# Optimization experiments

Measured on AMD Instinct MI355X. Metric: run time of the kernel, lower is better.

## Reference

```python
import jax, jax.numpy as jnp
import numpy as np
from jax import lax

PRE_NMS_TOPN = 6000
POST_NMS_TOPN = 300
NMS_IOU = 0.7
VARIANCES = np.array([0.1, 0.1, 0.2, 0.2], dtype=np.float32)


def setup_inputs() -> dict:
    key = jax.random.key(0)
    k1, k2, k3, k4 = jax.random.split(key, 4)
    B, FH, FW, K = 32, 128, 128, 9
    A = FH * FW * K  # 147456 total anchors
    rpn_bbox_deltas = jax.random.normal(k1, (B, A, 4), dtype=jnp.float32) * 0.1
    rpn_labels = jax.random.normal(k2, (B, FH, FW, K), dtype=jnp.float32)
    # Anchors in [y1, x1, y2, x2] with y1<y2, x1<x2 on a ~1024px image.
    ctr = jax.random.uniform(k3, (A, 2), dtype=jnp.float32) * 1024.0
    wh = jax.random.uniform(k4, (A, 2), dtype=jnp.float32) * 224.0 + 32.0
    anchors = jnp.concatenate([ctr - 0.5 * wh, ctr + 0.5 * wh], axis=-1)
    return {"rpn_bbox_deltas": rpn_bbox_deltas, "rpn_labels": rpn_labels, "anchors": anchors}


def get_bboxes_from_deltas(anchors, deltas):
    # anchors: [A, 4] (y1,x1,y2,x2); deltas: [B, A, 4] (dy,dx,dh,dw)
    anc_w = anchors[..., 3] - anchors[..., 1]
    anc_h = anchors[..., 2] - anchors[..., 0]
    anc_cx = anchors[..., 1] + 0.5 * anc_w
    anc_cy = anchors[..., 0] + 0.5 * anc_h
    bb_w = jnp.exp(deltas[..., 3]) * anc_w
    bb_h = jnp.exp(deltas[..., 2]) * anc_h
    bb_cx = deltas[..., 1] * anc_w + anc_cx
    bb_cy = deltas[..., 0] * anc_h + anc_cy
    y1 = bb_cy - 0.5 * bb_h
    x1 = bb_cx - 0.5 * bb_w
    y2 = bb_h + y1
    x2 = bb_w + x1
    return jnp.stack([y1, x1, y2, x2], axis=-1)


def nms_per_image(boxes, scores, iou_threshold, num_keep):
    # boxes: [N, 4] sorted by descending score; scores: [N]
    y1, x1, y2, x2 = boxes[:, 0], boxes[:, 1], boxes[:, 2], boxes[:, 3]
    areas = (y2 - y1) * (x2 - x1)

    def step(scores_rem, _):
        idx = jnp.argmax(scores_rem)
        valid = jnp.isfinite(scores_rem[idx])
        b = boxes[idx]
        iy1 = jnp.maximum(b[0], y1)
        ix1 = jnp.maximum(b[1], x1)
        iy2 = jnp.minimum(b[2], y2)
        ix2 = jnp.minimum(b[3], x2)
        inter = jnp.clip(iy2 - iy1, 0.0) * jnp.clip(ix2 - ix1, 0.0)
        b_area = (b[2] - b[0]) * (b[3] - b[1])
        iou = inter / (areas + b_area - inter + 1e-9)
        # IoU(box, itself) == 1 > threshold, so the picked box is also suppressed.
        new_scores = jnp.where(iou > iou_threshold, -jnp.inf, scores_rem)
        return new_scores, (idx, valid)

    _, (keep_idx, valid) = lax.scan(step, scores, None, length=num_keep)
    vf = valid.astype(boxes.dtype)
    keep_boxes = boxes[keep_idx] * vf[:, None]  # zero-pad invalid slots
    keep_scores = scores[keep_idx] * vf
    return keep_boxes, keep_scores


def reference(rpn_bbox_deltas, rpn_labels, anchors):
    A = anchors.shape[0]
    B = rpn_bbox_deltas.shape[0]
    deltas = rpn_bbox_deltas.reshape(B, A, 4) * jnp.asarray(VARIANCES)
    labels = jax.nn.softmax(rpn_labels, axis=-1).reshape(B, A)
    rpn_bboxes = get_bboxes_from_deltas(anchors, deltas)  # [B, A, 4]
    # top-k pre-NMS filter (lax.top_k output is already sorted descending)
    pre_scores, pre_idx = lax.top_k(labels, PRE_NMS_TOPN)  # [B, P]
    pre_boxes = jnp.take_along_axis(rpn_bboxes, pre_idx[..., None], axis=1)  # [B, P, 4]
    nms_fn = lambda b, s: nms_per_image(b, s, NMS_IOU, POST_NMS_TOPN)
    roi_bboxes, roi_scores = jax.vmap(nms_fn)(pre_boxes, pre_scores)
    return roi_bboxes, roi_scores
```

## Files before the change

kernel.cpp:

```cpp
#include <hip/hip_runtime.h>
#include <cstdint>
#include <cstddef>

#pragma clang fp contract(off)

#define KCLS 9
#define PRE_N 6000
#define POST_N 300
#define NMS_IOU_T 0.7f
#define HIST_BLOCK 256
#define CHUNKS_PER_IMG 32
#define NMS_BLOCK 512
#define NSEG 8
#define SEG_CAP 2048
#define RANK_LDS 8192

#define SUPP(pb, pa, mbx, mar, out) \
    bool out; { \
        float iy1_ = fmaxf((pb).x, (mbx).x); \
        float ix1_ = fmaxf((pb).y, (mbx).y); \
        float iy2_ = fminf((pb).z, (mbx).z); \
        float ix2_ = fminf((pb).w, (mbx).w); \
        float ih_ = iy2_ - iy1_; ih_ = ih_ > 0.f ? ih_ : 0.f; \
        float iw_ = ix2_ - ix1_; iw_ = iw_ > 0.f ? iw_ : 0.f; \
        float inter_ = ih_ * iw_; \
        float den_ = (mar) + (pa) - inter_ + 1e-9f; \
        float hi_ = 0.7000007f * den_; \
        float lo_ = 0.6999993f * den_; \
        out = inter_ > hi_; \
        if (inter_ >= lo_ && inter_ <= hi_) out = (inter_ / den_) > NMS_IOU_T; \
    }

__device__ __forceinline__ void pick_dev(
        const unsigned int* __restrict__ gh,
        int shift, int bins,
        unsigned int prefix_in, unsigned int krem_in,
        unsigned int* cnt,
        unsigned int* ssum,
        unsigned int* out) {
    const int t = threadIdx.x;
    const int per = bins >> 8;
    unsigned int my = 0;
    if (t < 256) {
        for (int i = 0; i < per; ++i) {
            unsigned int c = gh[t * per + i];
            cnt[t * per + i] = c;
            my += c;
        }
        ssum[t] = my;
    }
    __syncthreads();
    for (int d = 1; d < 256; d <<= 1) {
        unsigned int v = 0u;
        if (t < 256 && t + d < 256) v = ssum[t + d];
        __syncthreads();
        if (t < 256) ssum[t] += v;
        __syncthreads();
    }
    if (t < 256) {
        unsigned int above = ssum[t] - my;
        if (above < krem_in && ssum[t] >= krem_in) {
            unsigned int cum = above;
            for (int b = per - 1; b >= 0; --b) {
                unsigned int c = cnt[t * per + b];
                if (cum + c >= krem_in) {
                    out[0] = prefix_in | ((unsigned int)(t * per + b) << shift);
                    out[1] = krem_in - cum;
                    break;
                }
                cum += c;
            }
        }
    }
    __syncthreads();
}

__global__ void __launch_bounds__(256)
softmax_hist_kernel(const float* __restrict__ labels,
                    float* __restrict__ scores,
                    unsigned int* __restrict__ ghist,
                    int gpi) {
    __shared__ float buf[256 * KCLS];
    __shared__ unsigned int h[2048 * 4];
    const int tid = threadIdx.x;
    for (int i = tid; i < 2048 * 4; i += 256) h[i] = 0u;

    const size_t gbase = (size_t)blockIdx.x * (256 * KCLS);
    const float4* lin4 = (const float4*)(labels + gbase);
    float4* b4 = (float4*)buf;
    for (int i = tid; i < 576; i += 256) b4[i] = lin4[i];
    __syncthreads();

    const int sub = tid & 3;
    float v[KCLS];
    float m = -1e30f;
    #pragma unroll
    for (int k = 0; k < KCLS; ++k) { v[k] = buf[tid * KCLS + k]; m = fmaxf(m, v[k]); }
    float e[KCLS];
    float s = 0.f;
    #pragma unroll
    for (int k = 0; k < KCLS; ++k) { e[k] = expf(v[k] - m); s += e[k]; }
    #pragma unroll
    for (int k = 0; k < KCLS; ++k) {
        float r = e[k] / s;
        buf[tid * KCLS + k] = r;
        atomicAdd(&h[(((__float_as_uint(r) >> 21) & 2047u) << 2) | sub], 1u);
    }
    __syncthreads();

    float4* o4 = (float4*)(scores + gbase);
    for (int i = tid; i < 576; i += 256) o4[i] = b4[i];

    const int img0 = (blockIdx.x * 256) / gpi;
    unsigned int* gh = ghist + (size_t)img0 * 2048;
    for (int i = tid; i < 2048; i += 256) {
        unsigned int c = h[4 * i] + h[4 * i + 1] + h[4 * i + 2] + h[4 * i + 3];
        if (c) atomicAdd(&gh[i], c);
    }
}

__global__ void __launch_bounds__(HIST_BLOCK)
hist2_kernel(const float* __restrict__ scores,
             const unsigned int* __restrict__ ghist1,
             unsigned int* __restrict__ ghist2,
             int A) {
    __shared__ unsigned int h[2048];
    __shared__ unsigned int ssum[256];
    __shared__ unsigned int pk[2];
    const int img = blockIdx.y;
    const int chunk = blockIdx.x;
    const int tid = threadIdx.x;

    pick_dev(ghist1 + (size_t)img * 2048, 21, 2048, 0u, (unsigned)PRE_N, h, ssum, pk);
    const unsigned int prefix = pk[0];

    for (int i = tid; i < 2048; i += HIST_BLOCK) h[i] = 0u;
    __syncthreads();
    const int per = A / CHUNKS_PER_IMG;
    const float* sc = scores + (size_t)img * A + (size_t)chunk * per;
    for (int i = tid; i < per; i += HIST_BLOCK) {
        unsigned int v = __float_as_uint(sc[i]);
        if ((v & 0xFFE00000u) == prefix)
            atomicAdd(&h[(v >> 10) & 2047u], 1u);
    }
    __syncthreads();
    unsigned int* gh = ghist2 + (size_t)img * 2048;
    for (int i = tid; i < 2048; i += HIST_BLOCK) {
        unsigned int c = h[i];
        if (c) atomicAdd(&gh[i], c);
    }
}

#define CE(a, b, u) { if ((v[a] > v[b]) == (u)) { unsigned long long t_ = v[a]; v[a] = v[b]; v[b] = t_; } }
#define REG3(u) { CE(0,4,u) CE(1,5,u) CE(2,6,u) CE(3,7,u) \
                  CE(0,2,u) CE(1,3,u) CE(4,6,u) CE(5,7,u) \
                  CE(0,1,u) CE(2,3,u) CE(4,5,u) CE(6,7,u) }

__global__ void __launch_bounds__(512)
compact_sort_kernel(const float* __restrict__ scores,
                    const unsigned int* __restrict__ ghist1,
                    const unsigned int* __restrict__ ghist2,
                    unsigned long long* __restrict__ pool,
                    unsigned int* __restrict__ counts,
                    int A) {
    __shared__ unsigned long long lin[SEG_CAP];
    __shared__ unsigned int plo[2][SEG_CAP];
    __shared__ unsigned int phi[2][SEG_CAP];
    __shared__ unsigned int ssum[256];
    __shared__ unsigned int pk[2];
    __shared__ unsigned int cnt;
    const int img = blockIdx.y;
    const int seg = blockIdx.x;
    const int tid = threadIdx.x;
    const int lane = tid & 63;
    const int w = tid >> 6;
    const float* sc = scores + (size_t)img * A;

    unsigned int* cnt32 = (unsigned int*)lin;
    pick_dev(ghist1 + (size_t)img * 2048, 21, 2048, 0u, (unsigned)PRE_N, cnt32, ssum, pk);
    const unsigned int p1 = pk[0];
    const unsigned int k1 = pk[1];
    pick_dev(ghist2 + (size_t)img * 2048, 10, 2048, p1, k1, cnt32, ssum, pk);
    const unsigned int T = pk[0];

    if (tid == 0) cnt = 0u;
    for (int i = tid; i < SEG_CAP; i += 512) lin[i] = ~0ull;
    __syncthreads();

    const int ngr = A >> 6;
    const int nj = ngr / NSEG;
    for (int j = w; j < nj; j += 8) {
        int g = seg + j * NSEG;
        int i = (g << 6) + lane;
        unsigned int sv = __float_as_uint(sc[i]);
        bool push = (sv >= T);
        unsigned long long bal = __ballot(push ? 1 : 0);
        if (push) {
            int leader = __ffsll(bal) - 1;
            int rank = __popcll(bal & ((1ull << lane) - 1ull));
            unsigned int base = 0;
            if (lane == leader) base = atomicAdd(&cnt, (unsigned int)__popcll(bal));
            base = (unsigned int)__shfl((int)base, leader);
            unsigned int pos = base + (unsigned int)rank;
            if (pos < SEG_CAP)
                lin[pos] = (((unsigned long long)(~sv)) << 32) | (unsigned long long)(unsigned int)i;
        }
    }
    __syncthreads();

    int n = (int)cnt; if (n > SEG_CAP) n = SEG_CAP;
    int P2 = 512; while (P2 < n) P2 <<= 1;
    const int NT = P2 >> 3;
    const int t = tid;
    const bool act = (t < NT);

    unsigned long long v[8];
    if (act) {
        #pragma unroll
        for (int e = 0; e < 8; ++e) v[e] = lin[(t << 3) + e];
        CE(0,1,true) CE(2,3,false) CE(4,5,true) CE(6,7,false)
        CE(0,2,true) CE(1,3,true) CE(4,6,false) CE(5,7,false)
        CE(0,1,true) CE(2,3,true) CE(4,5,false) CE(6,7,false)
        bool u8 = ((t & 1) == 0);
        REG3(u8)
    }
    int b = 0;
    for (int k = 16; k <= P2; k <<= 1) {
        const bool up = (((t << 3) & k) == 0);
        for (int j = k >> 1; j >= 8; j >>= 1) {
            const int c = j >> 3;
            if (act) {
                #pragma unroll
                for (int e = 0; e < 8; ++e) {
                    int idx = e * NT + t;
                    plo[b][idx] = (unsigned int)v[e];
                    phi[b][idx] = (unsigned int)(v[e] >> 32);
                }
            }
            __syncthreads();
            if (act) {
                const int q = t ^ c;
                const bool keep_min = (up == ((t & c) == 0));
                #pragma unroll
                for (int e = 0; e < 8; ++e) {
                    int idx = e * NT + q;
                    unsigned long long wv = ((unsigned long long)phi[b][idx] << 32)
                                          | (unsigned long long)plo[b][idx];
                    bool less = v[e] < wv;
                    v[e] = (less == keep_min) ? v[e] : wv;
                }
            }
            b ^= 1;
        }
        if (act) { REG3(up) }
    }

    unsigned long long* gp = pool + ((size_t)img * NSEG + seg) * SEG_CAP;
    if (act) {
        #pragma unroll
        for (int e = 0; e < 8; ++e) {
            int r = (t << 3) + e;
            if (r < n) gp[r] = v[e];
        }
    }
    if (tid == 0) counts[img * NSEG + seg] = (unsigned int)n;
}

__global__ void __launch_bounds__(256)
rank_decode_kernel(const unsigned long long* __restrict__ pool,
                   const unsigned int* __restrict__ counts,
                   const float* __restrict__ deltas,
                   const float* __restrict__ anchors,
                   float* __restrict__ pre_boxes,
                   float* __restrict__ pre_scores,
                   int A) {
    __shared__ unsigned long long arr[RANK_LDS];
    const int img = blockIdx.y;
    const int seg = blockIdx.x;
    const int tid = threadIdx.x;

    int c[NSEG], off[NSEG + 1];
    const unsigned long long* gp[NSEG];
    off[0] = 0;
    #pragma unroll
    for (int s = 0; s < NSEG; ++s) {
        int cs = (int)counts[img * NSEG + s];
        if (cs > SEG_CAP) cs = SEG_CAP;
        c[s] = cs;
        off[s + 1] = off[s] + cs;
        gp[s] = pool + ((size_t)img * NSEG + s) * SEG_CAP;
    }
    const int total = off[NSEG];
    const bool inlds = (total <= RANK_LDS);
    if (inlds) {
        #pragma unroll
        for (int s = 0; s < NSEG; ++s)
            for (int i = tid; i < c[s]; i += 256) arr[off[s] + i] = gp[s][i];
    }
    __syncthreads();

    const int m = c[seg];
    for (int i = tid; i < m; i += 256) {
        unsigned long long key = inlds ? arr[off[seg] + i] : gp[seg][i];
        int pos = i;
        #pragma unroll
        for (int s = 0; s < NSEG; ++s) {
            if (s == seg) continue;
            const unsigned long long* base = inlds ? (arr + off[s]) : gp[s];
            int lo = 0, hi = c[s];
            while (lo < hi) {
                int mid = (lo + hi) >> 1;
                if (base[mid] < key) lo = mid + 1; else hi = mid;
            }
            pos += lo;
        }
        if (pos < PRE_N) {
            unsigned int bidx = (unsigned int)(key & 0xFFFFFFFFull);
            unsigned int sbits = ~((unsigned int)(key >> 32));
            float score = __uint_as_float(sbits);
            float a0 = anchors[(size_t)bidx * 4 + 0];
            float a1 = anchors[(size_t)bidx * 4 + 1];
            float a2 = anchors[(size_t)bidx * 4 + 2];
            float a3 = anchors[(size_t)bidx * 4 + 3];
            const float* dd = deltas + ((size_t)img * A + bidx) * 4;
            float d0 = dd[0] * 0.1f;
            float d1 = dd[1] * 0.1f;
            float d2 = dd[2] * 0.2f;
            float d3 = dd[3] * 0.2f;
            float anc_w = a3 - a1;
            float anc_h = a2 - a0;
            float anc_cx = a1 + 0.5f * anc_w;
            float anc_cy = a0 + 0.5f * anc_h;
            float bb_w = expf(d3) * anc_w;
            float bb_h = expf(d2) * anc_h;
            float bb_cx = d1 * anc_w + anc_cx;
            float bb_cy = d0 * anc_h + anc_cy;
            float y1 = bb_cy - 0.5f * bb_h;
            float x1 = bb_cx - 0.5f * bb_w;
            float y2 = bb_h + y1;
            float x2 = bb_w + x1;
            float* ob = pre_boxes + ((size_t)img * PRE_N + pos) * 4;
            ob[0] = y1; ob[1] = x1; ob[2] = y2; ob[3] = x2;
            pre_scores[(size_t)img * PRE_N + pos] = score;
        }
    }
}

__global__ void __launch_bounds__(NMS_BLOCK)
nms_kernel(const float* __restrict__ pre_boxes,
           const float* __restrict__ pre_scores,
           float* __restrict__ out_boxes,
           float* __restrict__ out_scores) {
    const int img = blockIdx.x;
    const int tid = threadIdx.x;
    const int lane = tid & 63;
    const int grp = tid >> 6;
    const float4* bb4 = (const float4*)(pre_boxes + (size_t)img * PRE_N * 4);

    __shared__ float4 kept[POST_N];
    __shared__ float  kept_area[POST_N];
    __shared__ int    kept_idx[POST_N];
    __shared__ float4 chunkbox[2][64];
    __shared__ unsigned long long rows[64];
    __shared__ unsigned long long supball[8];
    __shared__ int kept_cnt;

    const int NCH = (PRE_N + 63) >> 6;

    float4 nb = make_float4(0.f, 0.f, 0.f, 0.f);
    if (tid < 64) {
        chunkbox[0][tid] = bb4[tid];
        nb = bb4[64 + tid];
    }
    if (tid == 0) kept_cnt = 0;
    __syncthreads();

    for (int c = 0; c < NCH; ++c) {
        const int base = c << 6;
        const int cur = c & 1;
        const int K = kept_cnt;
        float4 mb = chunkbox[cur][lane];
        float marea = (mb.z - mb.x) * (mb.w - mb.y);

        bool sup = false;
        for (int k = grp; k < K; k += 8) {
            float4 pb = kept[k];
            float pa = kept_area[k];
            SUPP(pb, pa, mb, marea, s)
            if (s) { sup = true; break; }
        }
        unsigned long long bal = __ballot(sup ? 1 : 0);
        if (lane == 0) supball[grp] = bal;

        #pragma unroll
        for (int u = 0; u < 8; ++u) {
            const int i = (grp << 3) + u;
            float4 pb = chunkbox[cur][i];
            float pa = (pb.z - pb.x) * (pb.w - pb.y);
            SUPP(pb, pa, mb, marea, s)
            unsigned long long rb = __ballot(s ? 1 : 0);
            if (lane == 0) rows[i] = rb;
        }

        if (tid < 64) {
            chunkbox[cur ^ 1][tid] = nb;
            int j = base + 128 + tid;
            nb = (j < PRE_N) ? bb4[j] : make_float4(0.f, 0.f, 0.f, 0.f);
        }
        __syncthreads();

        if (grp == 0) {
            const int remn = PRE_N - base;
            unsigned long long ext = (remn >= 64) ? ~0ull : ((1ull << remn) - 1ull);
            unsigned long long sb = supball[0] | supball[1] | supball[2] | supball[3]
                                  | supball[4] | supball[5] | supball[6] | supball[7];
            unsigned long long rem = ext & ~sb;
            unsigned long long myrow = rows[lane];
            int kc = K;
            while (rem && kc < POST_N) {
                const int i = __ffsll(rem) - 1;
                if (lane == i) {
                    kept[kc] = mb;
                    kept_area[kc] = marea;
                    kept_idx[kc] = base + i;
                }
                unsigned long long ri = __shfl(myrow, i);
                rem &= ~(1ull << i);
                rem &= ~ri;
                ++kc;
            }
            if (lane == 0) kept_cnt = kc;
        }
        __syncthreads();
        if (kept_cnt >= POST_N) break;
    }

    const int kc = kept_cnt;
    for (int r = tid; r < kc; r += NMS_BLOCK) {
        float4 bx = kept[r];
        float* ob = out_boxes + ((size_t)img * POST_N + r) * 4;
        ob[0] = bx.x; ob[1] = bx.y; ob[2] = bx.z; ob[3] = bx.w;
        out_scores[(size_t)img * POST_N + r] =
            pre_scores[(size_t)img * PRE_N + kept_idx[r]];
    }
}

extern "C" void kernel_launch(void* const* d_in, const int* in_sizes, int n_in,
                              void* d_out, int out_size, void* d_ws, size_t ws_size,
                              hipStream_t stream) {
    const float* deltas  = (const float*)d_in[0];
    const float* labels  = (const float*)d_in[1];
    const float* anchors = (const float*)d_in[2];
    float* out = (float*)d_out;

    const int A = in_sizes[2] / 4;
    const int B = in_sizes[0] / (A * 4);
    const int ngroups = in_sizes[1] / KCLS;
    const int gpi = ngroups / B;

    float* scores     = (float*)d_ws;
    float* pre_boxes  = scores + (size_t)B * A;
    float* pre_scores = pre_boxes + (size_t)B * PRE_N * 4;
    unsigned int* hist  = (unsigned int*)(pre_scores + (size_t)B * PRE_N);
    unsigned long long* pool = (unsigned long long*)(hist + (size_t)2 * B * 2048);
    unsigned int* counts = (unsigned int*)(pool + (size_t)B * NSEG * SEG_CAP);

    unsigned int* ghist1 = hist;
    unsigned int* ghist2 = hist + (size_t)B * 2048;

    float* out_boxes  = out;
    float* out_scores = out + (size_t)B * POST_N * 4;

    hipMemsetAsync(d_out, 0, (size_t)out_size * sizeof(float), stream);
    hipMemsetAsync(hist, 0, (size_t)2 * B * 2048 * sizeof(unsigned int), stream);

    softmax_hist_kernel<<<ngroups / 256, 256, 0, stream>>>(labels, scores, ghist1, gpi);

    dim3 hgrid(CHUNKS_PER_IMG, B);
    hist2_kernel<<<hgrid, HIST_BLOCK, 0, stream>>>(scores, ghist1, ghist2, A);

    dim3 sgrid(NSEG, B);
    compact_sort_kernel<<<sgrid, 512, 0, stream>>>(scores, ghist1, ghist2, pool, counts, A);
    rank_decode_kernel<<<sgrid, 256, 0, stream>>>(pool, counts, deltas, anchors,
                                                  pre_boxes, pre_scores, A);

    nms_kernel<<<B, NMS_BLOCK, 0, stream>>>(pre_boxes, pre_scores, out_boxes, out_scores);
}
```

Before: 262.9 us.

## Overlap next chunk's intra-chunk IoU rows with serial greedy resolve

Moves the intra-chunk 64x64 suppression-matrix computation off the critical path. Waves 1-7 now build the rows for chunk c+1 and prefetch chunk c+2 while wave 0 does the serial greedy resolve for chunk c. The rows buffer is double-buffered, and chunk 0's rows are computed in a prologue. This shortens each loop iteration's critical path, at the cost of an extra buffer, an extra prologue barrier, and a deeper prefetch distance.

```diff
diff --git a/kernel.cpp b/kernel.cpp
--- a/kernel.cpp
+++ b/kernel.cpp
@@ -361,7 +361,7 @@
     __shared__ float  kept_area[POST_N];
     __shared__ int    kept_idx[POST_N];
     __shared__ float4 chunkbox[2][64];
-    __shared__ unsigned long long rows[64];
+    __shared__ unsigned long long rows[2][64];
     __shared__ unsigned long long supball[8];
     __shared__ int kept_cnt;
 
@@ -370,9 +370,24 @@
     float4 nb = make_float4(0.f, 0.f, 0.f, 0.f);
     if (tid < 64) {
         chunkbox[0][tid] = bb4[tid];
-        nb = bb4[64 + tid];
-    }
+        chunkbox[1][tid] = bb4[64 + tid];
+    }
+    if (grp == 1) nb = bb4[128 + lane];
     if (tid == 0) kept_cnt = 0;
+    __syncthreads();
+    {
+        float4 mb0 = chunkbox[0][lane];
+        float mar0 = (mb0.z - mb0.x) * (mb0.w - mb0.y);
+        #pragma unroll
+        for (int u = 0; u < 8; ++u) {
+            const int i = (grp << 3) + u;
+            float4 pb = chunkbox[0][i];
+            float pa = (pb.z - pb.x) * (pb.w - pb.y);
+            SUPP(pb, pa, mb0, mar0, s)
+            unsigned long long rb = __ballot(s ? 1 : 0);
+            if (lane == 0) rows[0][i] = rb;
+        }
+    }
     __syncthreads();
 
     for (int c = 0; c < NCH; ++c) {
@@ -391,22 +406,6 @@
         }
         unsigned long long bal = __ballot(sup ? 1 : 0);
         if (lane == 0) supball[grp] = bal;
-
-        #pragma unroll
-        for (int u = 0; u < 8; ++u) {
-            const int i = (grp << 3) + u;
-            float4 pb = chunkbox[cur][i];
-            float pa = (pb.z - pb.x) * (pb.w - pb.y);
-            SUPP(pb, pa, mb, marea, s)
-            unsigned long long rb = __ballot(s ? 1 : 0);
-            if (lane == 0) rows[i] = rb;
-        }
-
-        if (tid < 64) {
-            chunkbox[cur ^ 1][tid] = nb;
-            int j = base + 128 + tid;
-            nb = (j < PRE_N) ? bb4[j] : make_float4(0.f, 0.f, 0.f, 0.f);
-        }
         __syncthreads();
 
         if (grp == 0) {
@@ -415,7 +414,7 @@
             unsigned long long sb = supball[0] | supball[1] | supball[2] | supball[3]
                                   | supball[4] | supball[5] | supball[6] | supball[7];
             unsigned long long rem = ext & ~sb;
-            unsigned long long myrow = rows[lane];
+            unsigned long long myrow = rows[cur][lane];
             int kc = K;
             while (rem && kc < POST_N) {
                 const int i = __ffsll(rem) - 1;
@@ -430,6 +429,21 @@
                 ++kc;
             }
             if (lane == 0) kept_cnt = kc;
+        } else if (c + 1 < NCH) {
+            float4 mb2 = chunkbox[cur ^ 1][lane];
+            float mar2 = (mb2.z - mb2.x) * (mb2.w - mb2.y);
+            for (int i = grp - 1; i < 64; i += 7) {
+                float4 pb = chunkbox[cur ^ 1][i];
+                float pa = (pb.z - pb.x) * (pb.w - pb.y);
+                SUPP(pb, pa, mb2, mar2, s)
+                unsigned long long rb = __ballot(s ? 1 : 0);
+                if (lane == 0) rows[cur ^ 1][i] = rb;
+            }
+            if (grp == 1 && c + 2 < NCH) {
+                chunkbox[cur][lane] = nb;
+                int j = base + 192 + lane;
+                nb = (j < PRE_N) ? bb4[j] : make_float4(0.f, 0.f, 0.f, 0.f);
+            }
         }
         __syncthreads();
         if (kept_cnt >= POST_N) break;
```

Result: no change. 259.1 us (-1.5%).
